# Kernel tuning notes

Hardware: AMD Instinct MI355X
Metric: run time of the kernel (lower is better)

The kernel has to match this reference:

```python
import jax, jax.numpy as jnp
import numpy as np

NUM_HEADS = 8

def _avg_pool_3x3_s2(x):
    # x: [BN, H, W, C]; AvgPool2d(kernel=3, stride=2, padding=1, count_include_pad=True)
    s = jax.lax.reduce_window(x, 0.0, jax.lax.add, (1, 3, 3, 1), (1, 2, 2, 1),
                              [(0, 0), (1, 1), (1, 1), (0, 0)])
    return s / 9.0

def _rel_dist(q_size, k_size):
    q_ratio = max(k_size / q_size, 1.0)
    k_ratio = max(q_size / k_size, 1.0)
    d = np.arange(q_size)[:, None] * q_ratio - np.arange(k_size)[None, :] * k_ratio
    d += (k_size - 1) * k_ratio
    return jnp.asarray(d.astype(np.int32))

def setup_inputs() -> dict:
    key = jax.random.key(0)
    ks = jax.random.split(key, 8)
    B, C, H, W = 128, 1024, 24, 24
    hd = C // NUM_HEADS
    rel_dim = 2 * max(H // 2, H) - 1  # 47
    return {
        "x": jax.random.normal(ks[0], (B, C, H, W), jnp.float32),
        "Wq": jax.random.normal(ks[1], (C, C), jnp.float32) * 0.02,
        "Wk": jax.random.normal(ks[2], (C, C), jnp.float32) * 0.02,
        "Wv": jax.random.normal(ks[3], (C, C), jnp.float32) * 0.02,
        "Wp": jax.random.normal(ks[4], (C, C), jnp.float32) * 0.02,
        "bp": jnp.zeros((C,), jnp.float32),
        "rel_pos_h": jax.random.normal(ks[5], (rel_dim, hd), jnp.float32) * 0.02,
        "rel_pos_w": jax.random.normal(ks[6], (rel_dim, hd), jnp.float32) * 0.02,
    }

def reference(x, Wq, Wk, Wv, Wp, bp, rel_pos_h, rel_pos_w):
    B, C, H, W = x.shape
    nh = NUM_HEADS
    hd = C // nh
    N = H * W
    xt = x.reshape(B, C, N).transpose(0, 2, 1)            # [B, N, C]
    # pool_first: split into heads, avg-pool Q spatially (K, V unpooled)
    xh = xt.reshape(B, N, nh, hd).transpose(0, 2, 1, 3)   # [B, nh, N, hd]
    qp = _avg_pool_3x3_s2(xh.reshape(B * nh, H, W, hd))   # [B*nh, 12, 12, hd]
    qh, qw = qp.shape[1], qp.shape[2]
    qN = qh * qw
    # merge heads back, apply per-branch linears (no bias)
    q = qp.reshape(B, nh, qN, hd).transpose(0, 2, 1, 3).reshape(B, qN, C) @ Wq
    q = q.reshape(B, qN, nh, hd).transpose(0, 2, 1, 3)    # [B, nh, qN, hd]
    k = (xt @ Wk).reshape(B, N, nh, hd).transpose(0, 2, 1, 3)
    v = (xt @ Wv).reshape(B, N, nh, hd).transpose(0, 2, 1, 3)
    scale = hd ** -0.5
    attn = jnp.einsum('bhqd,bhkd->bhqk', q * scale, k)    # [B, nh, qN, N]
    # spatial relative position bias
    Rh = rel_pos_h[_rel_dist(qh, H)]                      # [qh, H, hd]
    Rw = rel_pos_w[_rel_dist(qw, W)]                      # [qw, W, hd]
    r_q = q.reshape(B, nh, qh, qw, hd)
    rel_h = jnp.einsum('byhwc,hkc->byhwk', r_q, Rh)       # [B, nh, qh, qw, H]
    rel_w = jnp.einsum('byhwc,wkc->byhwk', r_q, Rw)       # [B, nh, qh, qw, W]
    attn = (attn.reshape(B, nh, qh, qw, H, W)
            + rel_h[..., :, None] + rel_w[..., None, :]).reshape(B, nh, qN, N)
    attn = jax.nn.softmax(attn, axis=-1)
    out = jnp.einsum('bhqk,bhkd->bhqd', attn, v) + q      # residual pooling
    out = out.transpose(0, 2, 1, 3).reshape(B, qN, C) @ Wp + bp
    return out.reshape(B, qh, qw, C).transpose(0, 3, 1, 2)  # [B, C, 12, 12]
```

## Files before the change

### kernel.cpp

```cpp
#include <hip/hip_runtime.h>
#include <hip/hip_bf16.h>

using bf16 = __hip_bfloat16;
typedef __attribute__((ext_vector_type(8))) short short8;
typedef __attribute__((ext_vector_type(4))) short s16x4;
typedef __attribute__((ext_vector_type(4))) float f32x4;

#define MFMA(a,b,c) __builtin_amdgcn_mfma_f32_16x16x32_bf16(a, b, c, 0, 0, 0)

#define B_      128
#define C_      1024
#define NH      8
#define HD      128
#define HW      24
#define NTOK    576
#define QH      12
#define QN      144

static __device__ __forceinline__ float bf2f(bf16 v) { return __bfloat162float(v); }
static __device__ __forceinline__ bf16  f2bf(float v) { return __float2bfloat16(v); }
static __device__ __forceinline__ float s2f(short s) {
    return __uint_as_float(((unsigned)(unsigned short)s) << 16);
}
static __device__ __forceinline__ unsigned bfbits(float v) {
    bf16 t = f2bf(v);
    return (unsigned)*(unsigned short*)&t;
}

__device__ __forceinline__ void gll16(const bf16* src, bf16* dst_lds) {
    __builtin_amdgcn_global_load_lds(
        (__attribute__((address_space(1))) const unsigned int*)src,
        (__attribute__((address_space(3))) unsigned int*)dst_lds,
        16, 0, 0);
}

__global__ __launch_bounds__(256) void transpose_cvt(
    const float* __restrict__ in, bf16* __restrict__ out,
    int R, int Ccols, size_t ibs, size_t obs)
{
    __shared__ float tile[32][33];
    const float* ib = in + (size_t)blockIdx.z * ibs;
    bf16* ob = out + (size_t)blockIdx.z * obs;
    int c0 = blockIdx.x * 32, r0 = blockIdx.y * 32;
    int tx = threadIdx.x & 31, ty = threadIdx.x >> 5;
    #pragma unroll
    for (int i = 0; i < 32; i += 8)
        tile[ty + i][tx] = ib[(size_t)(r0 + ty + i) * Ccols + c0 + tx];
    __syncthreads();
    #pragma unroll
    for (int i = 0; i < 32; i += 8)
        ob[(size_t)(c0 + ty + i) * R + r0 + tx] = f2bf(tile[tx][ty + i]);
}

__global__ __launch_bounds__(256) void transpose_w4(
    const float* __restrict__ p0, const float* __restrict__ p1,
    const float* __restrict__ p2, const float* __restrict__ p3,
    bf16* __restrict__ out)
{
    __shared__ float tile[32][33];
    int z = blockIdx.z;
    const float* ib = (z == 0) ? p0 : (z == 1) ? p1 : (z == 2) ? p2 : p3;
    bf16* ob = out + (size_t)z * 1048576;
    int c0 = blockIdx.x * 32, r0 = blockIdx.y * 32;
    int tx = threadIdx.x & 31, ty = threadIdx.x >> 5;
    #pragma unroll
    for (int i = 0; i < 32; i += 8)
        tile[ty + i][tx] = ib[(size_t)(r0 + ty + i) * 1024 + c0 + tx];
    __syncthreads();
    #pragma unroll
    for (int i = 0; i < 32; i += 8)
        ob[(size_t)(c0 + ty + i) * 1024 + r0 + tx] = f2bf(tile[tx][ty + i]);
}

__global__ __launch_bounds__(256) void pool_kernel(const bf16* __restrict__ xt,
                                                   bf16* __restrict__ xp)
{
    int bqn = blockIdx.x;
    int b = bqn / QN, qn = bqn % QN;
    int y = qn / QH, x = qn % QH;
    int t = threadIdx.x;
    float s0 = 0, s1 = 0, s2 = 0, s3 = 0;
    for (int dy = 0; dy < 3; dy++) {
        int hy = 2 * y - 1 + dy;
        if (hy < 0 || hy >= HW) continue;
        for (int dx = 0; dx < 3; dx++) {
            int hx = 2 * x - 1 + dx;
            if (hx < 0 || hx >= HW) continue;
            const bf16* row = xt + (size_t)(b * NTOK + hy * HW + hx) * C_;
            s0 += bf2f(row[t]);
            s1 += bf2f(row[t + 256]);
            s2 += bf2f(row[t + 512]);
            s3 += bf2f(row[t + 768]);
        }
    }
    bf16* o = xp + (size_t)bqn * C_;
    const float n = 1.f / 9.f;
    o[t] = f2bf(s0 * n); o[t + 256] = f2bf(s1 * n);
    o[t + 512] = f2bf(s2 * n); o[t + 768] = f2bf(s3 * n);
}

template<int EPI, int GRP>
__global__ __launch_bounds__(256, 2) void gemm_nt(
    const bf16* __restrict__ A, const bf16* __restrict__ Bt,
    void* __restrict__ Cout, const float* __restrict__ bias)
{
    __shared__ bf16 lds[2][2][128 * 64];
    const int tid = threadIdx.x;
    const int wv = tid >> 6, ln = tid & 63;
    const int id = blockIdx.x;
    const int dm = id & 7, mid = (id >> 3) & 7, grp = id >> 6;
    const int mt = (GRP == 1) ? grp * 8 + dm : mid;
    const int nt = (GRP == 1) ? mid : grp * 8 + dm;
    const int m0 = mt * 128, n0 = nt * 128;
    const int wr = wv >> 1, wc = wv & 1;
    const int l15 = ln & 15, l4 = ln >> 4;
    const int r8 = ln >> 3, sl = ln & 7;
    const int sg = sl ^ r8;

    const bf16* gA = A + (size_t)m0 * C_;
    const bf16* gB = Bt + (size_t)n0 * C_;

    f32x4 zero = {0.f, 0.f, 0.f, 0.f};
    f32x4 acc[4][4];
    #pragma unroll
    for (int i = 0; i < 4; i++)
        #pragma unroll
        for (int j = 0; j < 4; j++) acc[i][j] = zero;

    auto stage = [&](int kt, int d) {
        const bf16* sa = gA + kt * 64;
        const bf16* sb = gB + kt * 64;
        bf16* la = lds[d][0];
        bf16* lb = lds[d][1];
        #pragma unroll
        for (int i = 0; i < 4; i++) {
            int chunk = wv * 4 + i;
            gll16(sa + (size_t)(chunk * 8 + r8) * C_ + sg * 8, la + chunk * 512);
            gll16(sb + (size_t)(chunk * 8 + r8) * C_ + sg * 8, lb + chunk * 512);
        }
    };

    stage(0, 0);
    asm volatile("s_waitcnt vmcnt(0)");
    __syncthreads();

    int cur = 0;
    for (int kt = 0; kt < 16; kt++) {
        if (kt < 15) stage(kt + 1, cur ^ 1);
        const bf16* la = lds[cur][0];
        const bf16* lb = lds[cur][1];
        #pragma unroll
        for (int ks = 0; ks < 2; ks++) {
            short8 af[4], bfr[4];
            #pragma unroll
            for (int fm = 0; fm < 4; fm++) {
                int row = wr * 64 + fm * 16 + l15;
                int slot = (ks * 4 + l4) ^ (row & 7);
                af[fm] = *(const short8*)((const char*)la + row * 128 + slot * 16);
            }
            #pragma unroll
            for (int fn = 0; fn < 4; fn++) {
                int row = wc * 64 + fn * 16 + l15;
                int slot = (ks * 4 + l4) ^ (row & 7);
                bfr[fn] = *(const short8*)((const char*)lb + row * 128 + slot * 16);
            }
            #pragma unroll
            for (int fm = 0; fm < 4; fm++)
                #pragma unroll
                for (int fn = 0; fn < 4; fn++)
                    acc[fm][fn] = MFMA(af[fm], bfr[fn], acc[fm][fn]);
        }
        asm volatile("s_waitcnt vmcnt(0)");
        __syncthreads();
        cur ^= 1;
    }

    #pragma unroll
    for (int fm = 0; fm < 4; fm++) {
        #pragma unroll
        for (int fn = 0; fn < 4; fn++) {
            #pragma unroll
            for (int r = 0; r < 4; r++) {
                int row = m0 + wr * 64 + fm * 16 + l4 * 4 + r;
                int col = n0 + wc * 64 + fn * 16 + l15;
                float v = acc[fm][fn][r];
                if constexpr (EPI == 0) {
                    ((bf16*)Cout)[(size_t)row * C_ + col] = f2bf(v);
                } else if constexpr (EPI == 2) {
                    int bb = col / QN, qn = col % QN;
                    ((float*)Cout)[(size_t)bb * (C_ * QN) + (size_t)row * QN + qn] =
                        v + bias[row];
                } else if constexpr (EPI == 3) {
                    int b = row / NTOK, n = row % NTOK;
                    int h = col >> 7, ci = col & 127;
                    int kt2 = n >> 5, kf = (n >> 4) & 1, klane = n & 15;
                    int ks2 = ci >> 5, chunk = (ci >> 3) & 3, e = ci & 7;
                    int lane = chunk * 16 + klane;
                    size_t addr = ((((size_t)(b * NH + h) * 18 + kt2) * 2 + kf) * 4 + ks2) * 512
                                  + lane * 8 + e;
                    ((bf16*)Cout)[addr] = f2bf(v);
                } else {
                    int b = col / NTOK, n = col % NTOK;
                    int h = row >> 7, ci = row & 127;
                    int hf = (ci >> 4) & 7, lanelo = ci & 15;
                    int kt2 = n >> 5, chunk = (n >> 3) & 3, e = n & 7;
                    int lane = chunk * 16 + lanelo;
                    size_t addr = (((size_t)(b * NH + h) * 18 + kt2) * 8 + hf) * 512
                                  + lane * 8 + e;
                    ((bf16*)Cout)[addr] = f2bf(v);
                }
            }
        }
    }
}

__global__ __launch_bounds__(256) void relcvt_kernel(
    const float* __restrict__ rph, const float* __restrict__ rpw,
    bf16* __restrict__ relph, bf16* __restrict__ relpw)
{
    int i = blockIdx.x * 256 + threadIdx.x;
    if (i < 6144) {
        bool v = i < 6016;
        relph[i] = v ? f2bf(rph[i]) : f2bf(0.f);
        relpw[i] = v ? f2bf(rpw[i]) : f2bf(0.f);
    }
}

__global__ __launch_bounds__(192) void relgemm_kernel(
    const bf16* __restrict__ qbuf, const bf16* __restrict__ relph,
    const bf16* __restrict__ relpw, bf16* __restrict__ rgh, bf16* __restrict__ rgw)
{
    const int bid = blockIdx.x;
    const int bh = bid / 3, qb = bid - bh * 3;
    const int b = bh >> 3, h = bh & 7;
    const int w = threadIdx.x >> 6, ln = threadIdx.x & 63;
    const int l15 = ln & 15, l4 = ln >> 4;
    const int qrow = qb * 48 + w * 16 + l15;
    const int y = qrow / 12, x = qrow - y * 12;

    short8 qfr[4];
    #pragma unroll
    for (int ks = 0; ks < 4; ks++)
        qfr[ks] = *(const short8*)(qbuf + (size_t)(b * QN + qrow) * C_ + h * HD +
                                   ks * 32 + l4 * 8);

    f32x4 zero = {0.f, 0.f, 0.f, 0.f};
    bf16* oh = rgh + (size_t)bh * (QN * 24);
    bf16* ow = rgw + (size_t)bh * (QN * 24);

    #pragma unroll
    for (int tile = 0; tile < 3; tile++) {
        short8 rfh[4], rfw[4];
        #pragma unroll
        for (int ks = 0; ks < 4; ks++) {
            rfh[ks] = *(const short8*)(relph + (tile * 16 + l15) * 128 + ks * 32 + l4 * 8);
            rfw[ks] = *(const short8*)(relpw + (tile * 16 + l15) * 128 + ks * 32 + l4 * 8);
        }
        f32x4 ah = zero, aw = zero;
        #pragma unroll
        for (int ks = 0; ks < 4; ks++) ah = MFMA(rfh[ks], qfr[ks], ah);
        #pragma unroll
        for (int ks = 0; ks < 4; ks++) aw = MFMA(rfw[ks], qfr[ks], aw);
        #pragma unroll
        for (int r = 0; r < 4; r++) {
            int d = tile * 16 + l4 * 4 + r;
            int kr = 2 * y + 23 - d;
            if (kr >= 0 && kr < 24) oh[qrow * 24 + kr] = f2bf(ah[r]);
            int kc = 2 * x + 23 - d;
            if (kc >= 0 && kc < 24) ow[qrow * 24 + kc] = f2bf(aw[r]);
        }
    }
}

__global__ __launch_bounds__(192) void attn_fused(
    const bf16* __restrict__ qbuf, const bf16* __restrict__ kfr,
    const bf16* __restrict__ vfr, const bf16* __restrict__ rgh,
    const bf16* __restrict__ rgw, bf16* __restrict__ attno)
{
    __shared__ bf16 relhL[QN * 24];
    __shared__ bf16 relwL[QN * 24];
    __shared__ bf16 kvlds[2][8192];
    __shared__ char plds[3][1024];

    const int bid = blockIdx.x;
    const int bh = ((bid & 7) * 128) + (bid >> 3);
    const int b = bh >> 3, h = bh & 7;
    const int w = threadIdx.x >> 6, ln = threadIdx.x & 63;
    const int l15 = ln & 15, l4 = ln >> 4;

    const bf16* kh = kfr + (size_t)bh * 18 * 4096;
    const bf16* vh = vfr + (size_t)bh * 18 * 4096;
    const bf16* qhb = qbuf + ((size_t)(b * QN) * C_ + h * HD);

    auto stage = [&](int kt, int d) {
        for (int c = w; c < 16; c += 3) {
            const bf16* src = (c < 8) ? (kh + (size_t)kt * 4096 + c * 512)
                                      : (vh + (size_t)kt * 4096 + (c - 8) * 512);
            gll16(src + ln * 8, &kvlds[d][c * 512]);
        }
    };

    stage(0, 0);

    {
        const short8* gh = (const short8*)(rgh + (size_t)bh * (QN * 24));
        const short8* gw = (const short8*)(rgw + (size_t)bh * (QN * 24));
        for (int i = threadIdx.x; i < 432; i += 192) {
            ((short8*)relhL)[i] = gh[i];
            ((short8*)relwL)[i] = gw[i];
        }
    }

    short8 qfr[3][4];
    #pragma unroll
    for (int s = 0; s < 3; s++)
        #pragma unroll
        for (int ks = 0; ks < 4; ks++)
            qfr[s][ks] = *(const short8*)(qhb + (size_t)(w * 48 + s * 16 + l15) * C_ +
                                          ks * 32 + l4 * 8);

    f32x4 zero = {0.f, 0.f, 0.f, 0.f};
    f32x4 Of[3][8];
    float ls[3] = {0.f, 0.f, 0.f};
    #pragma unroll
    for (int s = 0; s < 3; s++)
        #pragma unroll
        for (int hf = 0; hf < 8; hf++) Of[s][hf] = zero;

    const float scale = 0.08838834764831845f;
    const int xsw = (l15 >> 1) & 3;

    asm volatile("s_waitcnt vmcnt(0)");
    __syncthreads();

    int cur = 0;
    for (int kt = 0; kt < 18; kt++) {
        if (kt < 17) stage(kt + 1, cur ^ 1);
        const bf16* kbuf = &kvlds[cur][0];
        const bf16* vbuf = &kvlds[cur][4096];
        #pragma unroll
        for (int s = 0; s < 3; s++) {
            const int rb = (w * 48 + s * 16 + l15) * 24;
            f32x4 S[2];
            #pragma unroll
            for (int kf = 0; kf < 2; kf++) {
                f32x4 acc = zero;
                #pragma unroll
                for (int ks = 0; ks < 4; ks++) {
                    short8 kb = *(const short8*)(kbuf + (kf * 4 + ks) * 512 + ln * 8);
                    acc = MFMA(kb, qfr[s][ks], acc);
                }
                S[kf] = acc;
            }
            float p[8];
            #pragma unroll
            for (int kf = 0; kf < 2; kf++) {
                #pragma unroll
                for (int r = 0; r < 4; r++) {
                    int key = kt * 32 + kf * 16 + l4 * 4 + r;
                    int kr = key / 24, kc = key - kr * 24;
                    p[kf * 4 + r] = __expf(S[kf][r] * scale + bf2f(relhL[rb + kr]) +
                                           bf2f(relwL[rb + kc]));
                }
            }
            ls[s] += ((p[0] + p[1]) + (p[2] + p[3])) + ((p[4] + p[5]) + (p[6] + p[7]));
            #pragma unroll
            for (int kf = 0; kf < 2; kf++) {
                unsigned u0 = bfbits(p[kf * 4 + 0]) | (bfbits(p[kf * 4 + 1]) << 16);
                unsigned u1 = bfbits(p[kf * 4 + 2]) | (bfbits(p[kf * 4 + 3]) << 16);
                int s16 = (kf * 2 + (l4 >> 1)) ^ xsw;
                *(unsigned long long*)(&plds[w][l15 * 64 + s16 * 16 + (l4 & 1) * 8]) =
                    ((unsigned long long)u1 << 32) | u0;
            }
            short8 pf = *(const short8*)(&plds[w][l15 * 64 + (l4 ^ xsw) * 16]);
            #pragma unroll
            for (int hf = 0; hf < 8; hf++) {
                short8 vb = *(const short8*)(vbuf + hf * 512 + ln * 8);
                Of[s][hf] = MFMA(vb, pf, Of[s][hf]);
            }
        }
        asm volatile("s_waitcnt vmcnt(0)");
        __syncthreads();
        cur ^= 1;
    }

    #pragma unroll
    for (int s = 0; s < 3; s++) {
        float t = ls[s];
        t += __shfl_xor(t, 16, 64);
        t += __shfl_xor(t, 32, 64);
        float inv = 1.f / t;
        int qrow = w * 48 + s * 16 + l15;
        const bf16* qrb = qhb + (size_t)qrow * C_;
        bf16* orb = attno + ((size_t)(b * QN + qrow) * C_ + h * HD);
        #pragma unroll
        for (int hf = 0; hf < 8; hf++) {
            s16x4 qres = *(const s16x4*)(qrb + hf * 16 + l4 * 4);
            s16x4 o;
            #pragma unroll
            for (int r = 0; r < 4; r++) {
                float v = Of[s][hf][r] * inv + s2f(qres[r]);
                o[r] = (short)bfbits(v);
            }
            *(s16x4*)(orb + hf * 16 + l4 * 4) = o;
        }
    }
}

extern "C" void kernel_launch(void* const* d_in, const int* in_sizes, int n_in,
                              void* d_out, int out_size, void* d_ws, size_t ws_size,
                              hipStream_t stream)
{
    const float* x   = (const float*)d_in[0];
    const float* Wq  = (const float*)d_in[1];
    const float* Wk  = (const float*)d_in[2];
    const float* Wv  = (const float*)d_in[3];
    const float* Wp  = (const float*)d_in[4];
    const float* bp  = (const float*)d_in[5];
    const float* rph = (const float*)d_in[6];
    const float* rpw = (const float*)d_in[7];

    char* ws = (char*)d_ws;
    const size_t MB = 1024 * 1024;
    bf16* Wqt  = (bf16*)(ws + 0 * MB);
    bf16* Wkt  = (bf16*)(ws + 2 * MB);
    bf16* Wvt  = (bf16*)(ws + 4 * MB);
    bf16* Wpt  = (bf16*)(ws + 6 * MB);
    bf16* xt   = (bf16*)(ws + 8 * MB);
    bf16* rgh  = (bf16*)(ws + 8 * MB);
    bf16* rgw  = (bf16*)(ws + 16 * MB);
    bf16* relph = (bf16*)(ws + 24 * MB);
    bf16* relpw = (bf16*)(ws + 25 * MB);
    bf16* kfrb = (bf16*)(ws + 152 * MB);
    bf16* vfrb = (bf16*)(ws + 296 * MB);
    bf16* xp   = (bf16*)(ws + 440 * MB);
    bf16* qbuf = (bf16*)(ws + 476 * MB);
    bf16* attno = xp;

    transpose_w4<<<dim3(32, 32, 4), 256, 0, stream>>>(Wq, Wk, Wv, Wp, (bf16*)ws);
    transpose_cvt<<<dim3(18, 32, 128), 256, 0, stream>>>(
        x, xt, 1024, 576, (size_t)1024 * 576, (size_t)576 * 1024);
    pool_kernel<<<dim3(B_ * QN), 256, 0, stream>>>(xt, xp);
    gemm_nt<3, 1><<<dim3(4608), 256, 0, stream>>>(xt, Wkt, kfrb, nullptr);
    gemm_nt<4, 2><<<dim3(4608), 256, 0, stream>>>(Wvt, xt, vfrb, nullptr);
    gemm_nt<0, 1><<<dim3(1152), 256, 0, stream>>>(xp, Wqt, qbuf, nullptr);
    relcvt_kernel<<<dim3(24), 256, 0, stream>>>(rph, rpw, relph, relpw);
    relgemm_kernel<<<dim3(B_ * NH * 3), 192, 0, stream>>>(qbuf, relph, relpw, rgh, rgw);
    attn_fused<<<dim3(B_ * NH), 192, 0, stream>>>(qbuf, kfrb, vfrb, rgh, rgw, attno);
    gemm_nt<2, 2><<<dim3(1152), 256, 0, stream>>>(Wpt, attno, d_out, bp);
}
```

Before: 810.5 us.

## Use 256x256-tile 8-wave GEMM with interleaved staging for K and V projections

```diff
diff --git a/kernel.cpp b/kernel.cpp
--- a/kernel.cpp
+++ b/kernel.cpp
@@ -99,6 +99,35 @@
     o[t + 512] = f2bf(s2 * n); o[t + 768] = f2bf(s3 * n);
 }
 
+template<int EPI>
+__device__ __forceinline__ void epi_store(void* Cout, int row, int col, float v,
+                                          const float* bias) {
+    if constexpr (EPI == 0) {
+        ((bf16*)Cout)[(size_t)row * C_ + col] = f2bf(v);
+    } else if constexpr (EPI == 2) {
+        int bb = col / QN, qn = col % QN;
+        ((float*)Cout)[(size_t)bb * (C_ * QN) + (size_t)row * QN + qn] = v + bias[row];
+    } else if constexpr (EPI == 3) {
+        int b = row / NTOK, n = row % NTOK;
+        int h = col >> 7, ci = col & 127;
+        int kt2 = n >> 5, kf = (n >> 4) & 1, klane = n & 15;
+        int ks2 = ci >> 5, chunk = (ci >> 3) & 3, e = ci & 7;
+        int lane = chunk * 16 + klane;
+        size_t addr = ((((size_t)(b * NH + h) * 18 + kt2) * 2 + kf) * 4 + ks2) * 512
+                      + lane * 8 + e;
+        ((bf16*)Cout)[addr] = f2bf(v);
+    } else {
+        int b = col / NTOK, n = col % NTOK;
+        int h = row >> 7, ci = row & 127;
+        int hf = (ci >> 4) & 7, lanelo = ci & 15;
+        int kt2 = n >> 5, chunk = (n >> 3) & 3, e = n & 7;
+        int lane = chunk * 16 + lanelo;
+        size_t addr = (((size_t)(b * NH + h) * 18 + kt2) * 8 + hf) * 512
+                      + lane * 8 + e;
+        ((bf16*)Cout)[addr] = f2bf(v);
+    }
+}
+
 template<int EPI, int GRP>
 __global__ __launch_bounds__(256, 2) void gemm_nt(
     const bf16* __restrict__ A, const bf16* __restrict__ Bt,
@@ -176,42 +205,152 @@
     }
 
     #pragma unroll
-    for (int fm = 0; fm < 4; fm++) {
-        #pragma unroll
-        for (int fn = 0; fn < 4; fn++) {
-            #pragma unroll
-            for (int r = 0; r < 4; r++) {
-                int row = m0 + wr * 64 + fm * 16 + l4 * 4 + r;
-                int col = n0 + wc * 64 + fn * 16 + l15;
-                float v = acc[fm][fn][r];
-                if constexpr (EPI == 0) {
-                    ((bf16*)Cout)[(size_t)row * C_ + col] = f2bf(v);
-                } else if constexpr (EPI == 2) {
-                    int bb = col / QN, qn = col % QN;
-                    ((float*)Cout)[(size_t)bb * (C_ * QN) + (size_t)row * QN + qn] =
-                        v + bias[row];
-                } else if constexpr (EPI == 3) {
-                    int b = row / NTOK, n = row % NTOK;
-                    int h = col >> 7, ci = col & 127;
-                    int kt2 = n >> 5, kf = (n >> 4) & 1, klane = n & 15;
-                    int ks2 = ci >> 5, chunk = (ci >> 3) & 3, e = ci & 7;
-                    int lane = chunk * 16 + klane;
-                    size_t addr = ((((size_t)(b * NH + h) * 18 + kt2) * 2 + kf) * 4 + ks2) * 512
-                                  + lane * 8 + e;
-                    ((bf16*)Cout)[addr] = f2bf(v);
-                } else {
-                    int b = col / NTOK, n = col % NTOK;
-                    int h = row >> 7, ci = row & 127;
-                    int hf = (ci >> 4) & 7, lanelo = ci & 15;
-                    int kt2 = n >> 5, chunk = (n >> 3) & 3, e = n & 7;
-                    int lane = chunk * 16 + lanelo;
-                    size_t addr = (((size_t)(b * NH + h) * 18 + kt2) * 8 + hf) * 512
-                                  + lane * 8 + e;
-                    ((bf16*)Cout)[addr] = f2bf(v);
-                }
-            }
-        }
-    }
+    for (int fm = 0; fm < 4; fm++)
+        #pragma unroll
+        for (int fn = 0; fn < 4; fn++)
+            #pragma unroll
+            for (int r = 0; r < 4; r++)
+                epi_store<EPI>(Cout, m0 + wr * 64 + fm * 16 + l4 * 4 + r,
+                               n0 + wc * 64 + fn * 16 + l15, acc[fm][fn][r], bias);
+}
+
+template<int EPI, int GRP>
+__global__ __launch_bounds__(512) void gemm256(
+    const bf16* __restrict__ A, const bf16* __restrict__ Bt, void* __restrict__ Cout)
+{
+    __shared__ bf16 lds[2][32768];
+
+    const int tid = threadIdx.x;
+    const int wv = tid >> 6, ln = tid & 63;
+    const int wm = wv >> 2, wn = wv & 3;
+    const int l15 = ln & 15, l4 = ln >> 4;
+    const int r8 = ln >> 3, sg = (ln & 7) ^ r8;
+
+    const int id = blockIdx.x;
+    const int dm = id & 7, q4 = (id >> 3) & 3, gq = id >> 5;
+    const int mt = (GRP == 1) ? gq * 8 + dm : q4;
+    const int nt = (GRP == 1) ? q4 : gq * 8 + dm;
+    const size_t m0 = (size_t)mt * 256, n0 = (size_t)nt * 256;
+
+    const bf16* gA = A + m0 * C_;
+    const bf16* gB = Bt + n0 * C_;
+
+    f32x4 zero = {0.f, 0.f, 0.f, 0.f};
+    f32x4 acc[8][4];
+    #pragma unroll
+    for (int i = 0; i < 8; i++)
+        #pragma unroll
+        for (int j = 0; j < 4; j++) acc[i][j] = zero;
+
+    auto stage_part = [&](int t, int part) {
+        bf16* dst = &lds[t & 1][part * 8192];
+        const bf16* src = (part < 2) ? (gA + (size_t)(part * 128) * C_ + t * 64)
+                                     : (gB + (size_t)((part - 2) * 128) * C_ + t * 64);
+        #pragma unroll
+        for (int i = 0; i < 2; i++) {
+            int chunk = wv * 2 + i;
+            gll16(src + (size_t)(chunk * 8 + r8) * C_ + sg * 8, dst + chunk * 512);
+        }
+    };
+
+    #pragma unroll
+    for (int p = 0; p < 4; p++) stage_part(0, p);
+    asm volatile("s_waitcnt vmcnt(0)");
+    __syncthreads();
+
+    const int brow0 = (wn & 1) * 64;
+
+    for (int t = 0; t < 16; t++) {
+        const char* Abase = (const char*)&lds[t & 1][wm * 8192];
+        const char* Bbase = (const char*)&lds[t & 1][16384 + (wn >> 1) * 8192];
+        short8 Af[4][2], Bf[4][2];
+
+        #pragma unroll
+        for (int fm = 0; fm < 4; fm++)
+            #pragma unroll
+            for (int ks = 0; ks < 2; ks++) {
+                int r = fm * 16 + l15;
+                int slot = (ks * 4 + l4) ^ (r & 7);
+                Af[fm][ks] = *(const short8*)(Abase + r * 128 + slot * 16);
+            }
+        #pragma unroll
+        for (int fn = 0; fn < 4; fn++)
+            #pragma unroll
+            for (int ks = 0; ks < 2; ks++) {
+                int r = brow0 + fn * 16 + l15;
+                int slot = (ks * 4 + l4) ^ (r & 7);
+                Bf[fn][ks] = *(const short8*)(Bbase + r * 128 + slot * 16);
+            }
+        if (t < 15) stage_part(t + 1, 0);
+        __builtin_amdgcn_s_barrier();
+        __builtin_amdgcn_s_setprio(1);
+        #pragma unroll
+        for (int fm = 0; fm < 4; fm++)
+            #pragma unroll
+            for (int fn = 0; fn < 2; fn++)
+                #pragma unroll
+                for (int ks = 0; ks < 2; ks++)
+                    acc[fm][fn] = MFMA(Af[fm][ks], Bf[fn][ks], acc[fm][fn]);
+        __builtin_amdgcn_s_setprio(0);
+        __builtin_amdgcn_s_barrier();
+
+        if (t < 15) stage_part(t + 1, 1);
+        __builtin_amdgcn_s_barrier();
+        __builtin_amdgcn_s_setprio(1);
+        #pragma unroll
+        for (int fm = 0; fm < 4; fm++)
+            #pragma unroll
+            for (int fn = 2; fn < 4; fn++)
+                #pragma unroll
+                for (int ks = 0; ks < 2; ks++)
+                    acc[fm][fn] = MFMA(Af[fm][ks], Bf[fn][ks], acc[fm][fn]);
+        __builtin_amdgcn_s_setprio(0);
+        __builtin_amdgcn_s_barrier();
+
+        #pragma unroll
+        for (int fm = 0; fm < 4; fm++)
+            #pragma unroll
+            for (int ks = 0; ks < 2; ks++) {
+                int r = (fm + 4) * 16 + l15;
+                int slot = (ks * 4 + l4) ^ (r & 7);
+                Af[fm][ks] = *(const short8*)(Abase + r * 128 + slot * 16);
+            }
+        if (t < 15) stage_part(t + 1, 2);
+        __builtin_amdgcn_s_barrier();
+        __builtin_amdgcn_s_setprio(1);
+        #pragma unroll
+        for (int fm = 0; fm < 4; fm++)
+            #pragma unroll
+            for (int fn = 0; fn < 2; fn++)
+                #pragma unroll
+                for (int ks = 0; ks < 2; ks++)
+                    acc[fm + 4][fn] = MFMA(Af[fm][ks], Bf[fn][ks], acc[fm + 4][fn]);
+        __builtin_amdgcn_s_setprio(0);
+        __builtin_amdgcn_s_barrier();
+
+        if (t < 15) stage_part(t + 1, 3);
+        __builtin_amdgcn_s_barrier();
+        __builtin_amdgcn_s_setprio(1);
+        #pragma unroll
+        for (int fm = 0; fm < 4; fm++)
+            #pragma unroll
+            for (int fn = 2; fn < 4; fn++)
+                #pragma unroll
+                for (int ks = 0; ks < 2; ks++)
+                    acc[fm + 4][fn] = MFMA(Af[fm][ks], Bf[fn][ks], acc[fm + 4][fn]);
+        __builtin_amdgcn_s_setprio(0);
+        asm volatile("s_waitcnt vmcnt(0)");
+        __builtin_amdgcn_s_barrier();
+    }
+
+    #pragma unroll
+    for (int fm = 0; fm < 8; fm++)
+        #pragma unroll
+        for (int fn = 0; fn < 4; fn++)
+            #pragma unroll
+            for (int r = 0; r < 4; r++)
+                epi_store<EPI>(Cout, (int)m0 + wm * 128 + fm * 16 + l4 * 4 + r,
+                               (int)n0 + wn * 64 + fn * 16 + l15, acc[fm][fn][r], nullptr);
 }
 
 __global__ __launch_bounds__(256) void relcvt_kernel(
@@ -441,8 +580,8 @@
     transpose_cvt<<<dim3(18, 32, 128), 256, 0, stream>>>(
         x, xt, 1024, 576, (size_t)1024 * 576, (size_t)576 * 1024);
     pool_kernel<<<dim3(B_ * QN), 256, 0, stream>>>(xt, xp);
-    gemm_nt<3, 1><<<dim3(4608), 256, 0, stream>>>(xt, Wkt, kfrb, nullptr);
-    gemm_nt<4, 2><<<dim3(4608), 256, 0, stream>>>(Wvt, xt, vfrb, nullptr);
+    gemm256<3, 1><<<dim3(1152), 512, 0, stream>>>(xt, Wkt, kfrb);
+    gemm256<4, 2><<<dim3(1152), 512, 0, stream>>>(Wvt, xt, vfrb);
     gemm_nt<0, 1><<<dim3(1152), 256, 0, stream>>>(xp, Wqt, qbuf, nullptr);
     relcvt_kernel<<<dim3(24), 256, 0, stream>>>(rph, rpw, relph, relpw);
     relgemm_kernel<<<dim3(B_ * NH * 3), 192, 0, stream>>>(qbuf, relph, relpw, rgh, rgw);
```

After: 810.2 us. Within noise of the previous version (-0.0%).
